# Kernel tuning notes

Hardware: AMD Instinct MI355X
Metric: run time of the kernel (lower is better)

## Reference

```python
import jax, jax.numpy as jnp
import numpy as np

T_STEPS, N_GRID = 730, 8000
NEARZERO = 1e-5
# parameter bounds, order: tt ddf alpha beta stor retip fscn scx flz stot cgw resmax k1 k2 k3 k4 k5 k6
_BOUNDS = [(-3,5),(0,20),(0,1),(0,1),(0,5),(0,50),(0,1),(0,1),(0.005,0.995),(1,2000),(0,20),(1,300),(0,1),(1,5),(0,1),(0,1),(0,1),(0,1)]
_LO = jnp.array([b[0] for b in _BOUNDS], dtype=jnp.float32)
_HI = jnp.array([b[1] for b in _BOUNDS], dtype=jnp.float32)


def setup_inputs() -> dict:
    key = jax.random.key(0)
    kx, kp = jax.random.split(key)
    x = jax.random.uniform(kx, (T_STEPS, N_GRID, 3), dtype=jnp.float32)
    # scale forcings to physical ranges: prcp in [0,10) mm/d, tmean in [-2,6) C, pet in [0,5) mm/d
    x = x * jnp.array([10.0, 8.0, 5.0], dtype=jnp.float32) + jnp.array([0.0, -2.0, 0.0], dtype=jnp.float32)
    parameters = jax.random.normal(kp, (T_STEPS, N_GRID, 18), dtype=jnp.float32)
    return {"x": x, "parameters": parameters}


def _prms_forward(x, parameters):
    # static params: sigmoid of NN output at static_idx = warm_up - 1 = -1, scaled to bounds
    p = jax.nn.sigmoid(parameters[-1, :, :18])            # [N, 18]
    p = _LO + p * (_HI - _LO)
    p = p[:, :, None]                                      # [N, 18, 1]  (nmul = 1)
    (tt, ddf, alpha, beta, stor, retip, fscn, scx, flz, stot,
     cgw, resmax, k1, k2, k3, k4, k5, k6) = [p[:, i] for i in range(18)]
    scn = fscn * scx
    remx = (1.0 - flz) * stot
    smax = flz * stot

    Pm = x[:, :, 0:1]    # precipitation [T, N, 1]
    Tm = x[:, :, 1:2]    # mean temperature
    PETm = x[:, :, 2:3]  # potential ET

    n_grid = x.shape[1]
    s0 = jnp.full((n_grid, 1), 0.001, dtype=jnp.float32)
    init = (s0, s0, s0, s0, s0, s0, s0)  # snow, XIN, RSTOR, RECHR, SMAV, RES, GW

    def step(state, inp):
        snow, xin, rstor, rechr, smav, res, gw = state
        PRECIP, temp, Ep = inp
        # snow partition and melt (delta_t = 1)
        is_snow = (temp <= tt).astype(jnp.float32)
        flux_ps = PRECIP * is_snow
        flux_pr = PRECIP * (1.0 - is_snow)
        snow = snow + flux_ps
        flux_m = jnp.maximum(ddf * (temp - tt), 0.0)
        flux_m = jnp.minimum(flux_m, snow)
        snow = jnp.maximum(snow - flux_m, NEARZERO)
        # interception
        flux_pim = flux_pr * (1.0 - beta)
        flux_psm = flux_pr * beta
        flux_pby = flux_psm * (1.0 - alpha)
        flux_pin = flux_psm * alpha
        xin = xin + flux_pin
        flux_ptf = jnp.maximum(xin - stor, 0.0)
        xin = jnp.maximum(xin - flux_ptf, NEARZERO)
        flux_ein = jnp.minimum(Ep * beta, xin)
        xin = jnp.maximum(xin - flux_ein, NEARZERO)
        # impervious reservoir
        flux_mim = flux_m * (1.0 - beta)
        flux_msm = flux_m * beta
        rstor = rstor + flux_mim + flux_pim
        flux_sas = jnp.maximum(rstor - retip, 0.0)
        rstor = jnp.maximum(rstor - flux_sas, NEARZERO)
        flux_eim = jnp.minimum((1.0 - beta) * Ep, rstor)
        rstor = jnp.maximum(rstor - flux_eim, NEARZERO)
        # surface runoff / infiltration to recharge zone
        sro_lin = jnp.clip(scn + (scx - scn) * (rechr / remx), 0.0, 1.0)
        inflow = flux_msm + flux_ptf + flux_pby
        flux_sro = sro_lin * inflow
        flux_inf = inflow - flux_sro
        rechr = rechr + flux_inf
        flux_pc = jnp.maximum(rechr - remx, 0.0)
        rechr = rechr - flux_pc
        evap_max_a = jnp.maximum(rechr / remx * (Ep - flux_ein - flux_eim), 0.0)
        flux_ea = jnp.minimum(evap_max_a, rechr)
        rechr = jnp.maximum(rechr - flux_ea, NEARZERO)
        # lower soil moisture zone
        smav = smav + flux_pc
        flux_excs = jnp.maximum(smav - smax, 0.0)
        smav = smav - flux_excs
        transp = jnp.where(rechr < (Ep - flux_ein - flux_eim),
                           jnp.maximum(smav / smax * (Ep - flux_ein - flux_eim - flux_ea), 0.0),
                           jnp.zeros_like(smav))
        transp = jnp.minimum(transp, smav)
        smav = jnp.maximum(smav - transp, NEARZERO)
        # seepage and subsurface reservoir
        flux_sep = jnp.minimum(cgw, flux_excs)
        flux_qres = jnp.maximum(flux_excs - flux_sep, 0.0)
        res = res + flux_qres
        flux_gad = k1 * (res / resmax) ** k2
        flux_gad = jnp.minimum(flux_gad, res)
        res = jnp.maximum(res - flux_gad, NEARZERO)
        flux_ras = k3 * res + k4 * res * res
        flux_ras = jnp.minimum(flux_ras, res)
        res = jnp.maximum(res - flux_ras, NEARZERO)
        # groundwater
        gw = gw + flux_gad + flux_sep
        flux_bas = k5 * gw
        gw = jnp.maximum(gw - flux_bas, NEARZERO)
        flux_snk = k6 * gw
        gw = jnp.maximum(gw - flux_snk, NEARZERO)
        q = flux_sas + flux_sro + flux_bas + flux_ras
        return (snow, xin, rstor, rechr, smav, res, gw), q

    _, Q = jax.lax.scan(step, init, (Pm, Tm, PETm))
    return Q  # [T, N, 1]


def reference(x, parameters):
    return _prms_forward(x, parameters)
```

## Files before the change

### kernel.cpp

```cpp
#include <hip/hip_runtime.h>
#include <math.h>

#define T_STEPS 730
#define N_GRID  8000
#define NEARZERO 1e-5f

__constant__ float c_lo[18] = {-3.f, 0.f, 0.f, 0.f, 0.f, 0.f, 0.f, 0.f, 0.005f, 1.f,    0.f, 1.f,   0.f, 1.f, 0.f, 0.f, 0.f, 0.f};
__constant__ float c_hi[18] = { 5.f, 20.f, 1.f, 1.f, 5.f, 50.f, 1.f, 1.f, 0.995f, 2000.f, 20.f, 300.f, 1.f, 5.f, 1.f, 1.f, 1.f, 1.f};

#define EXP2F(v) __builtin_amdgcn_exp2f(v)
#define LOG2F(v) __builtin_amdgcn_logf(v)

constexpr int CH  = 10;
constexpr int NCH = T_STEPS / CH;

__global__ __launch_bounds__(128, 1) void prms_kernel(
    const float* __restrict__ x,
    const float* __restrict__ params,
    float* __restrict__ out)
{
    const int lane = threadIdx.x & 63;
    const int wv   = threadIdx.x >> 6;
    const int i    = blockIdx.x * 64 + lane;

    __shared__ float4 hx[2][CH][64];

    const float* pp = params + ((size_t)(T_STEPS - 1) * N_GRID + (size_t)i) * 18;
    float pr[18];
#pragma unroll
    for (int j = 0; j < 18; ++j) {
        float s = 1.0f / (1.0f + expf(-pp[j]));
        pr[j] = c_lo[j] + s * (c_hi[j] - c_lo[j]);
    }

    if (wv == 0) {
        const float tt = pr[0],  ddf = pr[1], alpha = pr[2], beta = pr[3];
        const float stor = pr[4], retip = pr[5];
        const float ombeta  = 1.0f - beta;
        const float omalpha = 1.0f - alpha;

        float snow = 0.001f, xin = 0.001f, rstor = 0.001f;

        float3 buf[CH];
#pragma unroll
        for (int u = 0; u < CH; ++u) {
            const float* q = x + ((size_t)u * N_GRID + (size_t)i) * 3;
            buf[u] = make_float3(q[0], q[1], q[2]);
        }

        for (int c = 0; c <= NCH; ++c) {
            if (c < NCH) {
                float3 nbuf[CH];
                if (c + 1 < NCH) {
#pragma unroll
                    for (int u = 0; u < CH; ++u) {
                        const float* q = x + ((size_t)((c + 1) * CH + u) * N_GRID + (size_t)i) * 3;
                        nbuf[u] = make_float3(q[0], q[1], q[2]);
                    }
                }

#pragma unroll
                for (int u = 0; u < CH; ++u) {
                    const float PRECIP = buf[u].x;
                    const float temp   = buf[u].y;
                    const float Ep     = buf[u].z;

                    const bool  snowy     = (temp <= tt);
                    const float flux_ps   = snowy ? PRECIP : 0.0f;
                    const float flux_pr   = PRECIP - flux_ps;
                    const float m0        = fmaxf(ddf * (temp - tt), 0.0f);
                    const float ps_m      = flux_ps - m0;
                    const float flux_pim  = flux_pr * ombeta;
                    const float flux_psm  = flux_pr * beta;
                    const float flux_pby  = flux_psm * omalpha;
                    const float flux_pin  = flux_psm * alpha;
                    const float eb        = Ep * beta;
                    const float eim_cap   = ombeta * Ep;
                    const float pin_eb    = flux_pin - eb;
                    const float stor_eb   = stor - eb;
                    const float retip_eim = retip - eim_cap;

                    const float snow1  = snow + flux_ps;
                    const float flux_m = fminf(m0, snow1);
                    snow = fmaxf(snow + ps_m, NEARZERO);

                    const float xin1     = xin + flux_pin;
                    const float flux_ptf = fmaxf(xin1 - stor, 0.0f);
                    const float xin2     = fmaxf(fminf(xin1, stor), NEARZERO);
                    const float flux_ein = fminf(eb, xin2);
                    xin = fmaxf(fminf(xin + pin_eb, stor_eb), NEARZERO);

                    const float flux_mim = flux_m * ombeta;
                    const float rstor1   = rstor + (flux_mim + flux_pim);
                    const float flux_sas = fmaxf(rstor1 - retip, 0.0f);
                    const float rstor2   = fmaxf(fminf(rstor1, retip), NEARZERO);
                    const float flux_eim = fminf(eim_cap, rstor2);
                    rstor = fmaxf(fminf(rstor1 - eim_cap, retip_eim), NEARZERO);

                    const float flux_msm = flux_m * beta;
                    const float inflow   = flux_msm + (flux_ptf + flux_pby);
                    const float ep_rem   = Ep - flux_ein - flux_eim;
                    hx[c & 1][u][lane] = make_float4(inflow, ep_rem, flux_sas, 0.0f);
                }

                if (c + 1 < NCH) {
                    float3 nbuf[CH];
#pragma unroll
                    for (int u = 0; u < CH; ++u) {
                        const float* q = x + ((size_t)((c + 1) * CH + u) * N_GRID + (size_t)i) * 3;
                        nbuf[u] = make_float3(q[0], q[1], q[2]);
                    }
#pragma unroll
                    for (int u = 0; u < CH; ++u) buf[u] = nbuf[u];
                }
            }
            __syncthreads();
        }
    } else {
        const float fscn = pr[6], scx = pr[7], flz = pr[8], stot = pr[9];
        const float cgw = pr[10], resmax = pr[11];
        const float k1 = pr[12], k2 = pr[13], k3 = pr[14], k4 = pr[15];
        const float k5 = pr[16], k6 = pr[17];

        const float scn      = fscn * scx;
        const float remx     = (1.0f - flz) * stot;
        const float smax     = flz * stot;
        const float inv_remx = 1.0f / remx;
        const float inv_smax = 1.0f / smax;
        const float omscn    = 1.0f - scn;
        const float omk3     = 1.0f - k3;
        const float omk56    = (1.0f - k5) * (1.0f - k6);
        const float dscn     = (scx - scn) * inv_remx;
        const float pow_c2   = fmaf(k2, LOG2F(1.0f / resmax), LOG2F(k1));

        float rechr = 0.001f, smav = 0.001f, res = 0.001f, gw = 0.001f;

        for (int c = 0; c <= NCH; ++c) {
            if (c > 0) {
                const int cc = c - 1;
#pragma unroll
                for (int u = 0; u < CH; ++u) {
                    const float4 h = hx[cc & 1][u][lane];
                    const float inflow   = h.x;
                    const float ep_rem   = h.y;
                    const float flux_sas = h.z;

                    const float tkeep    = fminf(fmaxf(fmaf(-dscn, rechr, omscn), 0.0f), 1.0f);
                    const float flux_inf = inflow * tkeep;
                    const float flux_sro = inflow - flux_inf;

                    const float rechr1  = fmaf(inflow, tkeep, rechr);
                    const float flux_pc = fmaxf(rechr1 - remx, 0.0f);
                    const float rechr2  = fminf(rechr1, remx);
                    const float cfac    = inv_remx * ep_rem;
                    const float emax    = rechr2 * cfac;
                    const float flux_ea = fminf(emax, rechr2);
                    rechr = fmaxf(rechr2 * (1.0f - cfac), NEARZERO);

                    const float smav1     = smav + flux_pc;
                    const float flux_excs = fmaxf(smav1 - smax, 0.0f);
                    const float smav2     = fminf(smav1, smax);
                    const float gfac      = inv_smax * (ep_rem - flux_ea);
                    const float hkeep     = (rechr < ep_rem) ? (1.0f - gfac) : 1.0f;
                    smav = fmaxf(smav2 * hkeep, NEARZERO);

                    const float flux_sep  = fminf(cgw, flux_excs);
                    const float flux_qres = fmaxf(flux_excs - cgw, 0.0f);
                    const float res1      = res + flux_qres;
                    const float gad0      = EXP2F(fmaf(k2, LOG2F(res1), pow_c2));
                    const float flux_gad  = fminf(gad0, res1);
                    const float res2      = fmaxf(res1 - gad0, NEARZERO);
                    const float ras0      = fmaf(k4, res2, k3) * res2;
                    const float flux_ras  = fminf(ras0, res2);
                    res = fmaxf(res2 * fmaf(-k4, res2, omk3), NEARZERO);

                    const float gw1      = gw + (flux_gad + flux_sep);
                    const float flux_bas = k5 * gw1;
                    gw = fmaxf(gw1 * omk56, NEARZERO);

                    const float q = (flux_sas + flux_sro) + (flux_bas + flux_ras);
                    out[(size_t)(cc * CH + u) * N_GRID + (size_t)i] = q;
                }
            }
            __syncthreads();
        }
    }
}

extern "C" void kernel_launch(void* const* d_in, const int* in_sizes, int n_in,
                              void* d_out, int out_size, void* d_ws, size_t ws_size,
                              hipStream_t stream) {
    const float* x      = (const float*)d_in[0];
    const float* params = (const float*)d_in[1];
    float* out          = (float*)d_out;
    prms_kernel<<<dim3(N_GRID / 64), dim3(128), 0, stream>>>(x, params, out);
}
```

Before: 611.2 us.

## Split recurrence into four-wavefront pipeline with LDS handoff per stage

Extends the producer/consumer split from two wavefronts to four. Snow runs in one wave, interception in a second, soil in a third, and reservoir/groundwater in a fourth. Each wave hands chunked intermediates to the next through double-buffered shared memory, so the serial dependency chain per wave gets shorter and the stages overlap. The costs are extra LDS traffic, more barriers (three extra pipeline fill steps) and twice the threads per block.

```diff
diff --git a/kernel.cpp b/kernel.cpp
--- a/kernel.cpp
+++ b/kernel.cpp
@@ -14,7 +14,7 @@
 constexpr int CH  = 10;
 constexpr int NCH = T_STEPS / CH;
 
-__global__ __launch_bounds__(128, 1) void prms_kernel(
+__global__ __launch_bounds__(256, 1) void prms_kernel(
     const float* __restrict__ x,
     const float* __restrict__ params,
     float* __restrict__ out)
@@ -23,7 +23,10 @@
     const int wv   = threadIdx.x >> 6;
     const int i    = blockIdx.x * 64 + lane;
 
-    __shared__ float4 hx[2][CH][64];
+    __shared__ float4 c0a[2][CH][64];
+    __shared__ float4 c0b[2][CH][64];
+    __shared__ float4 c1 [2][CH][64];
+    __shared__ float2 c2 [2][CH][64];
 
     const float* pp = params + ((size_t)(T_STEPS - 1) * N_GRID + (size_t)i) * 18;
     float pr[18];
@@ -32,15 +35,27 @@
         float s = 1.0f / (1.0f + expf(-pp[j]));
         pr[j] = c_lo[j] + s * (c_hi[j] - c_lo[j]);
     }
+    const float tt = pr[0],  ddf = pr[1], alpha = pr[2], beta = pr[3];
+    const float stor = pr[4], retip = pr[5], fscn = pr[6], scx = pr[7];
+    const float flz = pr[8],  stot = pr[9], cgw = pr[10], resmax = pr[11];
+    const float k1 = pr[12],  k2 = pr[13], k3 = pr[14], k4 = pr[15];
+    const float k5 = pr[16],  k6 = pr[17];
+
+    const float ombeta   = 1.0f - beta;
+    const float omalpha  = 1.0f - alpha;
+    const float scn      = fscn * scx;
+    const float remx     = (1.0f - flz) * stot;
+    const float smax     = flz * stot;
+    const float inv_remx = 1.0f / remx;
+    const float inv_smax = 1.0f / smax;
+    const float omscn    = 1.0f - scn;
+    const float omk3     = 1.0f - k3;
+    const float omk56    = (1.0f - k5) * (1.0f - k6);
+    const float dscn     = (scx - scn) * inv_remx;
+    const float pow_c2   = fmaf(k2, LOG2F(1.0f / resmax), LOG2F(k1));
 
     if (wv == 0) {
-        const float tt = pr[0],  ddf = pr[1], alpha = pr[2], beta = pr[3];
-        const float stor = pr[4], retip = pr[5];
-        const float ombeta  = 1.0f - beta;
-        const float omalpha = 1.0f - alpha;
-
-        float snow = 0.001f, xin = 0.001f, rstor = 0.001f;
-
+        float snow = 0.001f;
         float3 buf[CH];
 #pragma unroll
         for (int u = 0; u < CH; ++u) {
@@ -48,10 +63,11 @@
             buf[u] = make_float3(q[0], q[1], q[2]);
         }
 
-        for (int c = 0; c <= NCH; ++c) {
+        for (int c = 0; c < NCH + 3; ++c) {
             if (c < NCH) {
                 float3 nbuf[CH];
-                if (c + 1 < NCH) {
+                const bool more = (c + 1 < NCH);
+                if (more) {
 #pragma unroll
                     for (int u = 0; u < CH; ++u) {
                         const float* q = x + ((size_t)((c + 1) * CH + u) * N_GRID + (size_t)i) * 3;
@@ -65,24 +81,53 @@
                     const float temp   = buf[u].y;
                     const float Ep     = buf[u].z;
 
-                    const bool  snowy     = (temp <= tt);
-                    const float flux_ps   = snowy ? PRECIP : 0.0f;
-                    const float flux_pr   = PRECIP - flux_ps;
-                    const float m0        = fmaxf(ddf * (temp - tt), 0.0f);
-                    const float ps_m      = flux_ps - m0;
-                    const float flux_pim  = flux_pr * ombeta;
-                    const float flux_psm  = flux_pr * beta;
-                    const float flux_pby  = flux_psm * omalpha;
-                    const float flux_pin  = flux_psm * alpha;
-                    const float eb        = Ep * beta;
-                    const float eim_cap   = ombeta * Ep;
+                    const bool  snowy    = (temp <= tt);
+                    const float flux_ps  = snowy ? PRECIP : 0.0f;
+                    const float flux_pr  = PRECIP - flux_ps;
+                    const float m0       = fmaxf(ddf * (temp - tt), 0.0f);
+                    const float ps_m     = flux_ps - m0;
+
+                    const float snow1  = snow + flux_ps;
+                    const float flux_m = fminf(m0, snow1);
+                    snow = fmaxf(snow + ps_m, NEARZERO);
+
+                    const float flux_pim = flux_pr * ombeta;
+                    const float flux_psm = flux_pr * beta;
+                    const float flux_pby = flux_psm * omalpha;
+                    const float flux_pin = flux_psm * alpha;
+                    const float eb       = Ep * beta;
+                    const float eim_cap  = ombeta * Ep;
+                    const float flux_mim = flux_m * ombeta;
+                    const float rin      = flux_mim + flux_pim;
+                    const float msm      = flux_m * beta;
+
+                    c0a[c & 1][u][lane] = make_float4(flux_pin, eb, rin, eim_cap);
+                    c0b[c & 1][u][lane] = make_float4(msm, flux_pby, Ep, 0.0f);
+                }
+
+                if (more) {
+#pragma unroll
+                    for (int u = 0; u < CH; ++u) buf[u] = nbuf[u];
+                }
+            }
+            __syncthreads();
+        }
+    } else if (wv == 1) {
+        float xin = 0.001f, rstor = 0.001f;
+
+        for (int c = 0; c < NCH + 3; ++c) {
+            const int cc = c - 1;
+            if (cc >= 0 && cc < NCH) {
+#pragma unroll
+                for (int u = 0; u < CH; ++u) {
+                    const float4 a = c0a[cc & 1][u][lane];
+                    const float4 b = c0b[cc & 1][u][lane];
+                    const float flux_pin = a.x, eb = a.y, rin = a.z, eim_cap = a.w;
+                    const float msm = b.x, pby = b.y, Ep = b.z;
+
                     const float pin_eb    = flux_pin - eb;
                     const float stor_eb   = stor - eb;
                     const float retip_eim = retip - eim_cap;
-
-                    const float snow1  = snow + flux_ps;
-                    const float flux_m = fminf(m0, snow1);
-                    snow = fmaxf(snow + ps_m, NEARZERO);
 
                     const float xin1     = xin + flux_pin;
                     const float flux_ptf = fmaxf(xin1 - stor, 0.0f);
@@ -90,60 +135,29 @@
                     const float flux_ein = fminf(eb, xin2);
                     xin = fmaxf(fminf(xin + pin_eb, stor_eb), NEARZERO);
 
-                    const float flux_mim = flux_m * ombeta;
-                    const float rstor1   = rstor + (flux_mim + flux_pim);
+                    const float rstor1   = rstor + rin;
                     const float flux_sas = fmaxf(rstor1 - retip, 0.0f);
                     const float rstor2   = fmaxf(fminf(rstor1, retip), NEARZERO);
                     const float flux_eim = fminf(eim_cap, rstor2);
                     rstor = fmaxf(fminf(rstor1 - eim_cap, retip_eim), NEARZERO);
 
-                    const float flux_msm = flux_m * beta;
-                    const float inflow   = flux_msm + (flux_ptf + flux_pby);
-                    const float ep_rem   = Ep - flux_ein - flux_eim;
-                    hx[c & 1][u][lane] = make_float4(inflow, ep_rem, flux_sas, 0.0f);
-                }
-
-                if (c + 1 < NCH) {
-                    float3 nbuf[CH];
-#pragma unroll
-                    for (int u = 0; u < CH; ++u) {
-                        const float* q = x + ((size_t)((c + 1) * CH + u) * N_GRID + (size_t)i) * 3;
-                        nbuf[u] = make_float3(q[0], q[1], q[2]);
-                    }
-#pragma unroll
-                    for (int u = 0; u < CH; ++u) buf[u] = nbuf[u];
-                }
-            }
-            __syncthreads();
-        }
-    } else {
-        const float fscn = pr[6], scx = pr[7], flz = pr[8], stot = pr[9];
-        const float cgw = pr[10], resmax = pr[11];
-        const float k1 = pr[12], k2 = pr[13], k3 = pr[14], k4 = pr[15];
-        const float k5 = pr[16], k6 = pr[17];
-
-        const float scn      = fscn * scx;
-        const float remx     = (1.0f - flz) * stot;
-        const float smax     = flz * stot;
-        const float inv_remx = 1.0f / remx;
-        const float inv_smax = 1.0f / smax;
-        const float omscn    = 1.0f - scn;
-        const float omk3     = 1.0f - k3;
-        const float omk56    = (1.0f - k5) * (1.0f - k6);
-        const float dscn     = (scx - scn) * inv_remx;
-        const float pow_c2   = fmaf(k2, LOG2F(1.0f / resmax), LOG2F(k1));
-
-        float rechr = 0.001f, smav = 0.001f, res = 0.001f, gw = 0.001f;
-
-        for (int c = 0; c <= NCH; ++c) {
-            if (c > 0) {
-                const int cc = c - 1;
-#pragma unroll
-                for (int u = 0; u < CH; ++u) {
-                    const float4 h = hx[cc & 1][u][lane];
-                    const float inflow   = h.x;
-                    const float ep_rem   = h.y;
-                    const float flux_sas = h.z;
+                    const float inflow = msm + (flux_ptf + pby);
+                    const float ep_rem = Ep - flux_ein - flux_eim;
+                    c1[cc & 1][u][lane] = make_float4(inflow, ep_rem, flux_sas, 0.0f);
+                }
+            }
+            __syncthreads();
+        }
+    } else if (wv == 2) {
+        float rechr = 0.001f, smav = 0.001f;
+
+        for (int c = 0; c < NCH + 3; ++c) {
+            const int cc = c - 2;
+            if (cc >= 0 && cc < NCH) {
+#pragma unroll
+                for (int u = 0; u < CH; ++u) {
+                    const float4 h = c1[cc & 1][u][lane];
+                    const float inflow = h.x, ep_rem = h.y, flux_sas = h.z;
 
                     const float tkeep    = fminf(fmaxf(fmaf(-dscn, rechr, omscn), 0.0f), 1.0f);
                     const float flux_inf = inflow * tkeep;
@@ -163,6 +177,23 @@
                     const float gfac      = inv_smax * (ep_rem - flux_ea);
                     const float hkeep     = (rechr < ep_rem) ? (1.0f - gfac) : 1.0f;
                     smav = fmaxf(smav2 * hkeep, NEARZERO);
+
+                    const float s2 = flux_sas + flux_sro;
+                    c2[cc & 1][u][lane] = make_float2(flux_excs, s2);
+                }
+            }
+            __syncthreads();
+        }
+    } else {
+        float res = 0.001f, gw = 0.001f;
+
+        for (int c = 0; c < NCH + 3; ++c) {
+            const int cc = c - 3;
+            if (cc >= 0 && cc < NCH) {
+#pragma unroll
+                for (int u = 0; u < CH; ++u) {
+                    const float2 h = c2[cc & 1][u][lane];
+                    const float flux_excs = h.x, s2 = h.y;
 
                     const float flux_sep  = fminf(cgw, flux_excs);
                     const float flux_qres = fmaxf(flux_excs - cgw, 0.0f);
@@ -178,7 +209,7 @@
                     const float flux_bas = k5 * gw1;
                     gw = fmaxf(gw1 * omk56, NEARZERO);
 
-                    const float q = (flux_sas + flux_sro) + (flux_bas + flux_ras);
+                    const float q = s2 + (flux_bas + flux_ras);
                     out[(size_t)(cc * CH + u) * N_GRID + (size_t)i] = q;
                 }
             }
@@ -193,5 +224,5 @@
     const float* x      = (const float*)d_in[0];
     const float* params = (const float*)d_in[1];
     float* out          = (float*)d_out;
-    prms_kernel<<<dim3(N_GRID / 64), dim3(128), 0, stream>>>(x, params, out);
+    prms_kernel<<<dim3(N_GRID / 64), dim3(256), 0, stream>>>(x, params, out);
 }
```

New measurement: 597.7 us. -2.2%, faster.
